# Optimization experiments

Measured on AMD Instinct MI355X. Metric: run time of the kernel, lower is better.

The kernel has to match this reference:

```python
import jax, jax.numpy as jnp
import numpy as np

B, T, I, H, L, C = 64, 512, 128, 512, 3, 5


def setup_inputs() -> dict:
    key = jax.random.key(0)
    ks = jax.random.split(key, 2 + 4 * L + 2)
    s = 1.0 / np.sqrt(H)  # PyTorch RNN init range
    inp = {"x": jax.random.normal(ks[0], (B, T, I), dtype=jnp.float32)}
    in_dims = [I] + [H] * (L - 1)
    for l in range(L):
        k0, k1, k2, k3 = ks[1 + 4 * l:5 + 4 * l]
        inp[f"W_ih{l}"] = jax.random.uniform(k0, (H, in_dims[l]), jnp.float32, -s, s)
        inp[f"W_hh{l}"] = jax.random.uniform(k1, (H, H), jnp.float32, -s, s)
        inp[f"b_ih{l}"] = jax.random.uniform(k2, (H,), jnp.float32, -s, s)
        inp[f"b_hh{l}"] = jax.random.uniform(k3, (H,), jnp.float32, -s, s)
    so = 1.0 / np.sqrt(H)
    inp["W_out"] = jax.random.uniform(ks[-2], (C, H), jnp.float32, -so, so)
    inp["b_out"] = jax.random.uniform(ks[-1], (C,), jnp.float32, -so, so)
    return inp


def _rnn_layer(xs, W_ih, W_hh, b_ih, b_hh):
    # xs: [B, T, D] -> hidden sequence [B, T, H], ReLU RNN recurrence
    h0 = jnp.zeros((xs.shape[0], W_hh.shape[0]), xs.dtype)
    xproj = jnp.einsum('btd,hd->bth', xs, W_ih) + (b_ih + b_hh)  # precompute input GEMM

    def step(h, xp_t):
        h = jax.nn.relu(xp_t + h @ W_hh.T)
        return h, h

    _, ys = jax.lax.scan(step, h0, jnp.swapaxes(xproj, 0, 1))  # scan over time
    return jnp.swapaxes(ys, 0, 1)


def reference(x, W_ih0, W_hh0, b_ih0, b_hh0, W_ih1, W_hh1, b_ih1, b_hh1,
              W_ih2, W_hh2, b_ih2, b_hh2, W_out, b_out):
    h = x
    for W_ih, W_hh, b_ih, b_hh in ((W_ih0, W_hh0, b_ih0, b_hh0),
                                   (W_ih1, W_hh1, b_ih1, b_hh1),
                                   (W_ih2, W_hh2, b_ih2, b_hh2)):
        h = _rnn_layer(h, W_ih, W_hh, b_ih, b_hh)
    # last timestep -> linear head: [B, C]
    return h[:, -1, :] @ W_out.T + b_out
```

## Files before the change

### kernel.cpp

```cpp
#include <hip/hip_runtime.h>

#define BB 64
#define TT 512
#define II 128
#define HH 512
#define CC 5

__global__ __launch_bounds__(256) void gemm_bias_kernel(
    const float* __restrict__ A, const float* __restrict__ W,
    const float* __restrict__ b1, const float* __restrict__ b2,
    float* __restrict__ out, int K)
{
    __shared__ float As[16][132];
    __shared__ float Bs[16][132];
    const int tid = threadIdx.x;
    const int bm = blockIdx.x;
    const int bn = blockIdx.y;
    const int tx = tid & 15;
    const int ty = tid >> 4;
    const int lr = tid >> 2;
    const int lk = (tid & 3) << 2;

    const float* Ab = A + (size_t)bm * 128 * K;
    const float* Wb = W + (size_t)bn * 128 * K;

    float acc[8][8];
#pragma unroll
    for (int i = 0; i < 8; ++i)
#pragma unroll
        for (int j = 0; j < 8; ++j) acc[i][j] = 0.f;

    for (int k0 = 0; k0 < K; k0 += 16) {
        float4 a0 = *(const float4*)(Ab + (size_t)lr * K + k0 + lk);
        float4 a1 = *(const float4*)(Ab + (size_t)(lr + 64) * K + k0 + lk);
        float4 w0 = *(const float4*)(Wb + (size_t)lr * K + k0 + lk);
        float4 w1 = *(const float4*)(Wb + (size_t)(lr + 64) * K + k0 + lk);
        __syncthreads();
        As[lk + 0][lr] = a0.x; As[lk + 1][lr] = a0.y; As[lk + 2][lr] = a0.z; As[lk + 3][lr] = a0.w;
        As[lk + 0][lr + 64] = a1.x; As[lk + 1][lr + 64] = a1.y; As[lk + 2][lr + 64] = a1.z; As[lk + 3][lr + 64] = a1.w;
        Bs[lk + 0][lr] = w0.x; Bs[lk + 1][lr] = w0.y; Bs[lk + 2][lr] = w0.z; Bs[lk + 3][lr] = w0.w;
        Bs[lk + 0][lr + 64] = w1.x; Bs[lk + 1][lr + 64] = w1.y; Bs[lk + 2][lr + 64] = w1.z; Bs[lk + 3][lr + 64] = w1.w;
        __syncthreads();
#pragma unroll
        for (int k = 0; k < 16; ++k) {
            float4 av0 = *(const float4*)&As[k][ty * 8];
            float4 av1 = *(const float4*)&As[k][ty * 8 + 4];
            float4 bv0 = *(const float4*)&Bs[k][tx * 8];
            float4 bv1 = *(const float4*)&Bs[k][tx * 8 + 4];
            float a[8] = {av0.x, av0.y, av0.z, av0.w, av1.x, av1.y, av1.z, av1.w};
            float b[8] = {bv0.x, bv0.y, bv0.z, bv0.w, bv1.x, bv1.y, bv1.z, bv1.w};
#pragma unroll
            for (int i = 0; i < 8; ++i)
#pragma unroll
                for (int j = 0; j < 8; ++j)
                    acc[i][j] = fmaf(a[i], b[j], acc[i][j]);
        }
    }

    const int nb = bn * 128 + tx * 8;
    float bias[8];
#pragma unroll
    for (int j = 0; j < 8; ++j) bias[j] = b1[nb + j] + b2[nb + j];
#pragma unroll
    for (int i = 0; i < 8; ++i) {
        const size_t m = (size_t)bm * 128 + ty * 8 + i;
        float4 o0 = {acc[i][0] + bias[0], acc[i][1] + bias[1], acc[i][2] + bias[2], acc[i][3] + bias[3]};
        float4 o1 = {acc[i][4] + bias[4], acc[i][5] + bias[5], acc[i][6] + bias[6], acc[i][7] + bias[7]};
        *(float4*)(out + m * HH + nb) = o0;
        *(float4*)(out + m * HH + nb + 4) = o1;
    }
}

__global__ __launch_bounds__(512)
__attribute__((amdgpu_waves_per_eu(2, 2)))
void scan_kernel(
    const float* __restrict__ xp, const float* __restrict__ Whh,
    float* __restrict__ y, unsigned int* hbuf)
{
    __shared__ float hb[2][2 * HH];
    __shared__ float part[2][8][2][64];

    const int tid  = threadIdx.x;
    const int s    = blockIdx.x >> 5;
    const int g    = blockIdx.x & 31;
    const int lane = tid & 63;
    const int wv   = tid >> 6;

    const float* wr = Whh + (size_t)(s * 64 + lane) * HH + wv * 64;
    const float4 w0  = *(const float4*)(wr + 0);
    const float4 w1  = *(const float4*)(wr + 4);
    const float4 w2  = *(const float4*)(wr + 8);
    const float4 w3  = *(const float4*)(wr + 12);
    const float4 w4  = *(const float4*)(wr + 16);
    const float4 w5  = *(const float4*)(wr + 20);
    const float4 w6  = *(const float4*)(wr + 24);
    const float4 w7  = *(const float4*)(wr + 28);
    const float4 w8  = *(const float4*)(wr + 32);
    const float4 w9  = *(const float4*)(wr + 36);
    const float4 w10 = *(const float4*)(wr + 40);
    const float4 w11 = *(const float4*)(wr + 44);
    const float4 w12 = *(const float4*)(wr + 48);
    const float4 w13 = *(const float4*)(wr + 52);
    const float4 w14 = *(const float4*)(wr + 56);
    const float4 w15 = *(const float4*)(wr + 60);

    hb[0][tid] = 0.f;
    hb[0][tid + 512] = 0.f;

    unsigned int* gbase = hbuf + (size_t)g * 2048;
    const int gb0 = g * 2, gb1 = g * 2 + 1;
    float xp0 = 0.f, xp1 = 0.f;
    if (wv == s) {
        xp0 = xp[(size_t)gb0 * TT * HH + s * 64 + lane];
        xp1 = xp[(size_t)gb1 * TT * HH + s * 64 + lane];
    }
    __syncthreads();

    for (int t = 0; t < TT; ++t) {
        const int p = t & 1;

        float a0 = 0.f, a1 = 0.f, b0 = 0.f, b1 = 0.f;
        const float* h0p = &hb[p][wv * 64];
        const float* h1p = &hb[p][512 + wv * 64];
#define STEP4(WQ, OFF)                                                   \
        {                                                                \
            float4 h0 = *(const float4*)(h0p + (OFF));                   \
            float4 h1 = *(const float4*)(h1p + (OFF));                   \
            a0 = fmaf(WQ.x, h0.x, a0); a1 = fmaf(WQ.y, h0.y, a1);        \
            a0 = fmaf(WQ.z, h0.z, a0); a1 = fmaf(WQ.w, h0.w, a1);        \
            b0 = fmaf(WQ.x, h1.x, b0); b1 = fmaf(WQ.y, h1.y, b1);        \
            b0 = fmaf(WQ.z, h1.z, b0); b1 = fmaf(WQ.w, h1.w, b1);        \
        }
        STEP4(w0, 0)   STEP4(w1, 4)   STEP4(w2, 8)   STEP4(w3, 12)
        STEP4(w4, 16)  STEP4(w5, 20)  STEP4(w6, 24)  STEP4(w7, 28)
        STEP4(w8, 32)  STEP4(w9, 36)  STEP4(w10, 40) STEP4(w11, 44)
        STEP4(w12, 48) STEP4(w13, 52) STEP4(w14, 56) STEP4(w15, 60)
#undef STEP4
        part[p][wv][0][lane] = a0 + a1;
        part[p][wv][1][lane] = b0 + b1;
        __syncthreads();

        const int q = t + 1;
        const int slot = q & 1;
        const unsigned int phase = (unsigned int)(((q + 1) >> 1) & 1);

        if (wv == s) {
            float s0 = 0.f, s1 = 0.f;
#pragma unroll
            for (int w = 0; w < 8; ++w) {
                s0 += part[p][w][0][lane];
                s1 += part[p][w][1][lane];
            }
            const float hn0 = fmaxf(s0 + xp0, 0.f);
            const float hn1 = fmaxf(s1 + xp1, 0.f);
            if (q < TT) {
                unsigned int* dst = gbase + slot * 1024 + s * 64 + lane;
                __hip_atomic_store(dst, __float_as_uint(hn0) | (phase << 31),
                                   __ATOMIC_RELAXED, __HIP_MEMORY_SCOPE_AGENT);
                __hip_atomic_store(dst + 512, __float_as_uint(hn1) | (phase << 31),
                                   __ATOMIC_RELAXED, __HIP_MEMORY_SCOPE_AGENT);
            }
            hb[p ^ 1][s * 64 + lane] = hn0;
            hb[p ^ 1][512 + s * 64 + lane] = hn1;
            y[((size_t)gb0 * TT + t) * HH + s * 64 + lane] = hn0;
            y[((size_t)gb1 * TT + t) * HH + s * 64 + lane] = hn1;
            if (q < TT) {
                xp0 = xp[((size_t)gb0 * TT + q) * HH + s * 64 + lane];
                xp1 = xp[((size_t)gb1 * TT + q) * HH + s * 64 + lane];
            }
        } else if (q < TT) {
            unsigned int* src = gbase + slot * 1024 + tid;
            unsigned int u0, u1;
            for (;;) {
                u0 = __hip_atomic_load(src, __ATOMIC_RELAXED, __HIP_MEMORY_SCOPE_AGENT);
                u1 = __hip_atomic_load(src + 512, __ATOMIC_RELAXED, __HIP_MEMORY_SCOPE_AGENT);
                if (((u0 >> 31) == phase) && ((u1 >> 31) == phase)) break;
            }
            hb[p ^ 1][tid] = __uint_as_float(u0 & 0x7fffffffu);
            hb[p ^ 1][512 + tid] = __uint_as_float(u1 & 0x7fffffffu);
        }
    }
}

__global__ __launch_bounds__(64) void head_kernel(
    const float* __restrict__ y2, const float* __restrict__ Wout,
    const float* __restrict__ bout, float* __restrict__ out)
{
    const int bc = blockIdx.x;
    const int b = bc / CC, c = bc % CC;
    const int lane = threadIdx.x;
    const float* yrow = y2 + ((size_t)b * TT + (TT - 1)) * HH;
    const float* wrow = Wout + (size_t)c * HH;
    float s = 0.f;
#pragma unroll
    for (int i = 0; i < HH / 64; ++i)
        s = fmaf(yrow[lane + 64 * i], wrow[lane + 64 * i], s);
#pragma unroll
    for (int off = 32; off > 0; off >>= 1) s += __shfl_down(s, off);
    if (lane == 0) out[bc] = s + bout[c];
}

extern "C" void kernel_launch(void* const* d_in, const int* in_sizes, int n_in,
                              void* d_out, int out_size, void* d_ws, size_t ws_size,
                              hipStream_t stream)
{
    const float* x = (const float*)d_in[0];
    const float* W_ih[3] = {(const float*)d_in[1], (const float*)d_in[5], (const float*)d_in[9]};
    const float* W_hh[3] = {(const float*)d_in[2], (const float*)d_in[6], (const float*)d_in[10]};
    const float* b_ih[3] = {(const float*)d_in[3], (const float*)d_in[7], (const float*)d_in[11]};
    const float* b_hh[3] = {(const float*)d_in[4], (const float*)d_in[8], (const float*)d_in[12]};
    const float* W_out = (const float*)d_in[13];
    const float* b_out = (const float*)d_in[14];
    float* out = (float*)d_out;

    float* ws   = (float*)d_ws;
    float* Y    = ws;
    float* XP   = ws + (size_t)BB * TT * HH;
    unsigned int* hbuf = (unsigned int*)(XP + (size_t)BB * TT * HH);

    const size_t hbuf_bytes = 32 * 2 * 1024 * sizeof(unsigned int);
    const dim3 ggrid(256, 4, 1);

    gemm_bias_kernel<<<ggrid, 256, 0, stream>>>(x, W_ih[0], b_ih[0], b_hh[0], XP, II);
    hipMemsetAsync(hbuf, 0, hbuf_bytes, stream);
    scan_kernel<<<256, 512, 0, stream>>>(XP, W_hh[0], Y, hbuf);
    gemm_bias_kernel<<<ggrid, 256, 0, stream>>>(Y, W_ih[1], b_ih[1], b_hh[1], XP, HH);
    hipMemsetAsync(hbuf, 0, hbuf_bytes, stream);
    scan_kernel<<<256, 512, 0, stream>>>(XP, W_hh[1], Y, hbuf);
    gemm_bias_kernel<<<ggrid, 256, 0, stream>>>(Y, W_ih[2], b_ih[2], b_hh[2], XP, HH);
    hipMemsetAsync(hbuf, 0, hbuf_bytes, stream);
    scan_kernel<<<256, 512, 0, stream>>>(XP, W_hh[2], Y, hbuf);
    head_kernel<<<BB * CC, 64, 0, stream>>>(Y, W_out, b_out, out);
}
```

Before: 2.867 ms.

## Reassign scan rows so each wave reduces via shuffles, dropping LDS partial sums

Remaps the recurrent matvec so each group of 8 lanes owns one output row and splits K in eight, reducing partial dot products with xor-shuffles instead of an LDS partial buffer and a mid-step barrier. Every wave now publishes its own rows and all threads poll the global exchange buffer, including their own block's values, writing into a padded LDS layout. This removes one __syncthreads and the serial reduction done by a single wave per step. In exchange every block waits on a global round-trip even for rows it computed itself, and LDS reads are strided by 68 floats per segment.

```diff
diff --git a/kernel.cpp b/kernel.cpp
--- a/kernel.cpp
+++ b/kernel.cpp
@@ -77,16 +77,18 @@
     const float* __restrict__ xp, const float* __restrict__ Whh,
     float* __restrict__ y, unsigned int* hbuf)
 {
-    __shared__ float hb[2][2 * HH];
-    __shared__ float part[2][8][2][64];
+    __shared__ float hbs[2][2][8 * 68];
 
     const int tid  = threadIdx.x;
     const int s    = blockIdx.x >> 5;
     const int g    = blockIdx.x & 31;
     const int lane = tid & 63;
     const int wv   = tid >> 6;
-
-    const float* wr = Whh + (size_t)(s * 64 + lane) * HH + wv * 64;
+    const int rloc = lane >> 3;
+    const int kseg = lane & 7;
+    const int R    = s * 64 + wv * 8 + rloc;
+
+    const float* wr = Whh + (size_t)R * HH + kseg * 64;
     const float4 w0  = *(const float4*)(wr + 0);
     const float4 w1  = *(const float4*)(wr + 4);
     const float4 w2  = *(const float4*)(wr + 8);
@@ -104,81 +106,81 @@
     const float4 w14 = *(const float4*)(wr + 56);
     const float4 w15 = *(const float4*)(wr + 60);
 
-    hb[0][tid] = 0.f;
-    hb[0][tid + 512] = 0.f;
-
     unsigned int* gbase = hbuf + (size_t)g * 2048;
     const int gb0 = g * 2, gb1 = g * 2 + 1;
+
+    const int lds_w = (tid >> 6) * 68 + (tid & 63);
+
+    hbs[0][0][lds_w] = 0.f;
+    hbs[0][1][lds_w] = 0.f;
+
+    const bool pub = (kseg == 0);
     float xp0 = 0.f, xp1 = 0.f;
-    if (wv == s) {
-        xp0 = xp[(size_t)gb0 * TT * HH + s * 64 + lane];
-        xp1 = xp[(size_t)gb1 * TT * HH + s * 64 + lane];
+    if (pub) {
+        xp0 = xp[(size_t)gb0 * TT * HH + R];
+        xp1 = xp[(size_t)gb1 * TT * HH + R];
     }
     __syncthreads();
 
     for (int t = 0; t < TT; ++t) {
         const int p = t & 1;
 
-        float a0 = 0.f, a1 = 0.f, b0 = 0.f, b1 = 0.f;
-        const float* h0p = &hb[p][wv * 64];
-        const float* h1p = &hb[p][512 + wv * 64];
+        float a0 = 0.f, a1 = 0.f, c0 = 0.f, c1 = 0.f;
+        const float* h0p = &hbs[p][0][kseg * 68];
+        const float* h1p = &hbs[p][1][kseg * 68];
 #define STEP4(WQ, OFF)                                                   \
         {                                                                \
             float4 h0 = *(const float4*)(h0p + (OFF));                   \
             float4 h1 = *(const float4*)(h1p + (OFF));                   \
             a0 = fmaf(WQ.x, h0.x, a0); a1 = fmaf(WQ.y, h0.y, a1);        \
             a0 = fmaf(WQ.z, h0.z, a0); a1 = fmaf(WQ.w, h0.w, a1);        \
-            b0 = fmaf(WQ.x, h1.x, b0); b1 = fmaf(WQ.y, h1.y, b1);        \
-            b0 = fmaf(WQ.z, h1.z, b0); b1 = fmaf(WQ.w, h1.w, b1);        \
+            c0 = fmaf(WQ.x, h1.x, c0); c1 = fmaf(WQ.y, h1.y, c1);        \
+            c0 = fmaf(WQ.z, h1.z, c0); c1 = fmaf(WQ.w, h1.w, c1);        \
         }
         STEP4(w0, 0)   STEP4(w1, 4)   STEP4(w2, 8)   STEP4(w3, 12)
         STEP4(w4, 16)  STEP4(w5, 20)  STEP4(w6, 24)  STEP4(w7, 28)
         STEP4(w8, 32)  STEP4(w9, 36)  STEP4(w10, 40) STEP4(w11, 44)
         STEP4(w12, 48) STEP4(w13, 52) STEP4(w14, 56) STEP4(w15, 60)
 #undef STEP4
-        part[p][wv][0][lane] = a0 + a1;
-        part[p][wv][1][lane] = b0 + b1;
-        __syncthreads();
+
+        float A = a0 + a1, Bv = c0 + c1;
+        A  += __shfl_xor(A, 1);  A  += __shfl_xor(A, 2);  A  += __shfl_xor(A, 4);
+        Bv += __shfl_xor(Bv, 1); Bv += __shfl_xor(Bv, 2); Bv += __shfl_xor(Bv, 4);
 
         const int q = t + 1;
-        const int slot = q & 1;
+        unsigned int* slotp = gbase + (q & 1) * 1024;
         const unsigned int phase = (unsigned int)(((q + 1) >> 1) & 1);
 
-        if (wv == s) {
-            float s0 = 0.f, s1 = 0.f;
-#pragma unroll
-            for (int w = 0; w < 8; ++w) {
-                s0 += part[p][w][0][lane];
-                s1 += part[p][w][1][lane];
-            }
-            const float hn0 = fmaxf(s0 + xp0, 0.f);
-            const float hn1 = fmaxf(s1 + xp1, 0.f);
+        if (pub) {
+            const float hn0 = fmaxf(A + xp0, 0.f);
+            const float hn1 = fmaxf(Bv + xp1, 0.f);
             if (q < TT) {
-                unsigned int* dst = gbase + slot * 1024 + s * 64 + lane;
-                __hip_atomic_store(dst, __float_as_uint(hn0) | (phase << 31),
+                __hip_atomic_store(slotp + R, __float_as_uint(hn0) | (phase << 31),
                                    __ATOMIC_RELAXED, __HIP_MEMORY_SCOPE_AGENT);
-                __hip_atomic_store(dst + 512, __float_as_uint(hn1) | (phase << 31),
+                __hip_atomic_store(slotp + 512 + R, __float_as_uint(hn1) | (phase << 31),
                                    __ATOMIC_RELAXED, __HIP_MEMORY_SCOPE_AGENT);
             }
-            hb[p ^ 1][s * 64 + lane] = hn0;
-            hb[p ^ 1][512 + s * 64 + lane] = hn1;
-            y[((size_t)gb0 * TT + t) * HH + s * 64 + lane] = hn0;
-            y[((size_t)gb1 * TT + t) * HH + s * 64 + lane] = hn1;
+            y[((size_t)gb0 * TT + t) * HH + R] = hn0;
+            y[((size_t)gb1 * TT + t) * HH + R] = hn1;
             if (q < TT) {
-                xp0 = xp[((size_t)gb0 * TT + q) * HH + s * 64 + lane];
-                xp1 = xp[((size_t)gb1 * TT + q) * HH + s * 64 + lane];
+                xp0 = xp[((size_t)gb0 * TT + q) * HH + R];
+                xp1 = xp[((size_t)gb1 * TT + q) * HH + R];
             }
-        } else if (q < TT) {
-            unsigned int* src = gbase + slot * 1024 + tid;
+        }
+
+        if (q < TT) {
+            unsigned int* s0 = slotp + tid;
+            unsigned int* s1 = slotp + 512 + tid;
             unsigned int u0, u1;
             for (;;) {
-                u0 = __hip_atomic_load(src, __ATOMIC_RELAXED, __HIP_MEMORY_SCOPE_AGENT);
-                u1 = __hip_atomic_load(src + 512, __ATOMIC_RELAXED, __HIP_MEMORY_SCOPE_AGENT);
+                u0 = __hip_atomic_load(s0, __ATOMIC_RELAXED, __HIP_MEMORY_SCOPE_AGENT);
+                u1 = __hip_atomic_load(s1, __ATOMIC_RELAXED, __HIP_MEMORY_SCOPE_AGENT);
                 if (((u0 >> 31) == phase) && ((u1 >> 31) == phase)) break;
             }
-            hb[p ^ 1][tid] = __uint_as_float(u0 & 0x7fffffffu);
-            hb[p ^ 1][512 + tid] = __uint_as_float(u1 & 0x7fffffffu);
-        }
+            hbs[q & 1][0][lds_w] = __uint_as_float(u0 & 0x7fffffffu);
+            hbs[q & 1][1][lds_w] = __uint_as_float(u1 & 0x7fffffffu);
+        }
+        __syncthreads();
     }
 }
 
```

Result: faster. 2.723 ms (-5.0%).
